# Kernel tuning notes

Measured on AMD Instinct MI355X. Metric: run time of the kernel, lower is better.

Reference implementation:

```python
import jax, jax.numpy as jnp
import numpy as np

B, S, F, E, H = 4, 2048, 512, 512, 8
DH = E // H


def setup_inputs() -> dict:
    key = jax.random.key(0)
    ks = jax.random.split(key, 8)
    sc = 1.0 / np.sqrt(F)
    return {
        "x": jax.random.normal(ks[0], (B, S, F), jnp.float32),
        "etype_emb": jax.random.normal(ks[1], (B, S, E), jnp.float32),
        "mask": jax.random.randint(ks[2], (B, S), 0, 2, jnp.int32),
        "Wq": jax.random.normal(ks[3], (F, E), jnp.float32) * sc,
        "bq": jnp.zeros((E,), jnp.float32),
        "Wk": jax.random.normal(ks[4], (F, E), jnp.float32) * sc,
        "bk": jnp.zeros((E,), jnp.float32),
        "Wv": jax.random.normal(ks[5], (F, E), jnp.float32) * sc,
        "bv": jnp.zeros((E,), jnp.float32),
    }


def _heads(t):
    # [B,S,E] -> [B,H,S,DH]; tf.split on last dim + concat on axis 1 == this reshape/transpose
    return t.reshape(B, S, H, DH).transpose(0, 2, 1, 3)


def reference(x, etype_emb, mask, Wq, bq, Wk, bk, Wv, bv):
    # Dropout is identity in inference mode (training=None)
    q = _heads(x @ Wq + bq + etype_emb)            # [B,H,S,DH]
    k = _heads(x @ Wk + bk)
    v = _heads(x @ Wv + bv)
    scores = jnp.einsum("bhqd,bhkd->bhqk", q, k) / jnp.sqrt(jnp.float32(DH))
    NEG = jnp.float32(-1e10)
    m = (mask == 1)
    # mask keys before softmax
    scores = jnp.where(m[:, None, None, :], scores, NEG)
    att = jax.nn.softmax(scores, axis=-1)
    # mask queries after softmax (zero out)
    att = jnp.where(m[:, None, :, None], att, jnp.float32(0.0))
    h = jnp.einsum("bhqk,bhkd->bhqd", att, v)       # [B,H,S,DH]
    return h.transpose(0, 2, 1, 3).reshape(B, S, E)
```

## Files before the change

### kernel.cpp

```cpp
#include <hip/hip_runtime.h>
#include <hip/hip_bf16.h>


typedef _Float16 f16x4 __attribute__((ext_vector_type(4)));
typedef _Float16 f16x8 __attribute__((ext_vector_type(8)));
typedef float f32x4 __attribute__((ext_vector_type(4)));

#define MFMA16(a, b, c) __builtin_amdgcn_mfma_f32_16x16x16f16((a), (b), (c), 0, 0, 0)
#define MFMA32(a, b, c) __builtin_amdgcn_mfma_f32_16x16x32_f16((a), (b), (c), 0, 0, 0)
#define GLDS16(g, l)                                                                     \
    __builtin_amdgcn_global_load_lds((const __attribute__((address_space(1))) void*)(g), \
                                     (__attribute__((address_space(3))) void*)(l), 16, 0, 0)

constexpr int Bn = 4, Sn = 2048, Fn = 512, En = 512, Hn = 8, DHn = 64;

__global__ void cvt_f32_to_f16(const float* __restrict__ in, _Float16* __restrict__ out, int n4) {
    int i = blockIdx.x * blockDim.x + threadIdx.x;
    int stride = gridDim.x * blockDim.x;
    for (; i < n4; i += stride) {
        float4 v = reinterpret_cast<const float4*>(in)[i];
        f16x4 o = { (_Float16)v.x, (_Float16)v.y, (_Float16)v.z, (_Float16)v.w };
        reinterpret_cast<f16x4*>(out)[i] = o;
    }
}

__global__ void cvt_wT(const float* __restrict__ Wq, const float* __restrict__ Wk,
                       const float* __restrict__ Wv, _Float16* __restrict__ out) {
    const int z = blockIdx.z;
    const float* W = (z == 0) ? Wq : ((z == 1) ? Wk : Wv);
    _Float16* o = out + (size_t)z * Fn * En;
    __shared__ float tile[16][17];
    int n = blockIdx.x * 16 + threadIdx.x;
    int k = blockIdx.y * 16 + threadIdx.y;
    tile[threadIdx.y][threadIdx.x] = W[k * En + n];
    __syncthreads();
    int n2 = blockIdx.x * 16 + threadIdx.y;
    int k2 = blockIdx.y * 16 + threadIdx.x;
    o[(size_t)n2 * Fn + k2] = (_Float16)tile[threadIdx.x][threadIdx.y];
}

__global__ __launch_bounds__(256) void qkv_gemm(
    const _Float16* __restrict__ xh, const _Float16* __restrict__ wT,
    const float* __restrict__ bq, const float* __restrict__ bk, const float* __restrict__ bv,
    char* __restrict__ Qh, char* __restrict__ Kpk, char* __restrict__ Vpk) {
    const int z = blockIdx.z;
    const _Float16* Wz = wT + (size_t)z * Fn * En;
    const float* bias = (z == 0) ? bq : ((z == 1) ? bk : bv);

    const int tid = threadIdx.x;
    const int wave = tid >> 6, lane = tid & 63;
    const int lr = lane & 15, hi = lane >> 4;
    const int wr = wave >> 1, wc = wave & 1;
    const int m0 = blockIdx.x * 128;
    const int n0 = blockIdx.y * 128;

    __shared__ __align__(16) char smem[34816];
    char* As = smem;
    char* Bs = smem + 16384;

    f32x4 acc[4][4] = {};

    const int inrow = (tid & 7) * 16;
    const int rowb = tid >> 3;

    const char* xg = (const char*)xh;
    const char* wg = (const char*)Wz;

    for (int t = 0; t < 8; ++t) {
        const int k0b = t * 128;
        __syncthreads();
#pragma unroll
        for (int it = 0; it < 4; ++it) {
            const int row = rowb + it * 32;
            const int srccol = inrow ^ ((row & 7) << 4);
            const char* ga = xg + (size_t)(m0 + row) * 1024 + k0b + srccol;
            const char* gb = wg + (size_t)(n0 + row) * 1024 + k0b + srccol;
            const int ldso = (it * 256 + tid) * 16;
            GLDS16(ga, As + ldso);
            GLDS16(gb, Bs + ldso);
        }
        asm volatile("s_waitcnt vmcnt(0)" ::: "memory");
        __syncthreads();
#pragma unroll
        for (int ks = 0; ks < 2; ++ks) {
            f16x8 af[4], bf[4];
            const int kb = ks * 64 + hi * 16;
#pragma unroll
            for (int mt = 0; mt < 4; ++mt) {
                const int row = wr * 64 + mt * 16 + lr;
                af[mt] = *reinterpret_cast<const f16x8*>(As + row * 128 + (kb ^ ((row & 7) << 4)));
            }
#pragma unroll
            for (int nt = 0; nt < 4; ++nt) {
                const int row = wc * 64 + nt * 16 + lr;
                bf[nt] = *reinterpret_cast<const f16x8*>(Bs + row * 128 + (kb ^ ((row & 7) << 4)));
            }
#pragma unroll
            for (int mt = 0; mt < 4; ++mt)
#pragma unroll
                for (int nt = 0; nt < 4; ++nt)
                    acc[mt][nt] = MFMA32(af[mt], bf[nt], acc[mt][nt]);
        }
    }

    __syncthreads();
    _Float16* tl = (_Float16*)smem;
    {
        const int cb = wc * 64 + lr;
#pragma unroll
        for (int mt = 0; mt < 4; ++mt) {
            const int sb = wr * 64 + mt * 16 + hi * 4;
#pragma unroll
            for (int nt = 0; nt < 4; ++nt) {
                const int c = cb + nt * 16;
                const float bz = bias[n0 + c];
#pragma unroll
                for (int r = 0; r < 4; ++r)
                    tl[(sb + r) * 136 + c] = (_Float16)(acc[mt][nt][r] + bz);
            }
        }
    }
    __syncthreads();

    const int b8 = (m0 >> 11) * 8;
    const int h0 = n0 >> 6;
    const int kt0 = (m0 & 2047) >> 6;
    char* outz = (z == 0) ? Qh : ((z == 1) ? Kpk : Vpk);

#pragma unroll
    for (int chunk = 0; chunk < 4; ++chunk) {
        const int hh = chunk >> 1, T = chunk & 1;
        char* base = outz + (size_t)(b8 + h0 + hh) * 262144 + (size_t)(kt0 + T) * 8192;
#pragma unroll
        for (int j = 0; j < 2; ++j) {
            const int g = tid * 16 + j * 4096;
            f16x8 val;
            if (z == 0) {
                const int s = T * 64 + (g >> 7), db = g & 127;
                val = *reinterpret_cast<const f16x8*>(&tl[s * 136 + hh * 64 + (db >> 1)]);
            } else if (z == 1) {
                const int r = g >> 7;
                const int colb = (g & 127) ^ ((r & 7) << 4);
                val = *reinterpret_cast<const f16x8*>(&tl[(T * 64 + r) * 136 + hh * 64 + (colb >> 1)]);
            } else {
                const int d = g >> 7;
                const int k0 = ((g & 127) ^ ((d & 7) << 4)) >> 1;
#pragma unroll
                for (int jj = 0; jj < 8; ++jj)
                    val[jj] = tl[(T * 64 + k0 + jj) * 136 + hh * 64 + d];
            }
            *reinterpret_cast<f16x8*>(base + g) = val;
        }
    }
}

__global__ __launch_bounds__(256, 4) void attn(
    const _Float16* __restrict__ Qh, const char* __restrict__ Kpk,
    const char* __restrict__ Vpk, const int* __restrict__ mask,
    const float* __restrict__ etype, float* __restrict__ out) {
    const int bid = blockIdx.x;
    const int bh = bid & 31, qb = bid >> 5;
    const int b = bh >> 3, h = bh & 7;
    const int tid = threadIdx.x;
    const int wave = tid >> 6, lane = tid & 63;
    const int lr = lane & 15, hi = lane >> 4;
    const int q0 = qb * 64 + wave * 16;

    const _Float16* Qb = Qh + (size_t)bh * Sn * DHn;
    const char* Kb = Kpk + (size_t)bh * 262144;
    const char* Vb = Vpk + (size_t)bh * 262144;
    const int* mb = mask + b * Sn;

    constexpr float CSC = 0.18033688011112042f;
    constexpr int NT = Sn / 64;

    __shared__ __align__(16) char kv[2][16384];

#pragma unroll
    for (int j = 0; j < 2; ++j) {
        GLDS16(Kb + tid * 16 + j * 4096, kv[0] + tid * 16 + j * 4096);
        GLDS16(Vb + tid * 16 + j * 4096, kv[0] + 8192 + tid * 16 + j * 4096);
    }

    f16x8 qf[2];
#pragma unroll
    for (int ks = 0; ks < 2; ++ks) {
        const f16x8 qh = *reinterpret_cast<const f16x8*>(Qb + (q0 + lr) * DHn + ks * 32 + hi * 8);
        const float* ep = etype + ((size_t)(b * Sn) + q0 + lr) * En + h * DHn + ks * 32 + hi * 8;
        const f32x4 e0 = *reinterpret_cast<const f32x4*>(ep);
        const f32x4 e1 = *reinterpret_cast<const f32x4*>(ep + 4);
        f16x8 q;
#pragma unroll
        for (int j = 0; j < 4; ++j) q[j] = (_Float16)(((float)qh[j] + e0[j]) * CSC);
#pragma unroll
        for (int j = 0; j < 4; ++j) q[4 + j] = (_Float16)(((float)qh[4 + j] + e1[j]) * CSC);
        qf[ks] = q;
    }

    f32x4 oaccT[4] = {};
    f32x4 osum = {};
    float mrun = -3e38f;
    const f16x4 onev = {(_Float16)1.f, (_Float16)1.f, (_Float16)1.f, (_Float16)1.f};

    asm volatile("s_waitcnt vmcnt(0)" ::: "memory");
    __syncthreads();

    for (int t = 0; t < NT; ++t) {
        const char* cbuf = kv[t & 1];
        char* nbuf = kv[(t + 1) & 1];

        const size_t nto = (size_t)((t + 1) & (NT - 1)) * 8192;
#pragma unroll
        for (int j = 0; j < 2; ++j) {
            GLDS16(Kb + nto + tid * 16 + j * 4096, nbuf + tid * 16 + j * 4096);
            GLDS16(Vb + nto + tid * 16 + j * 4096, nbuf + 8192 + tid * 16 + j * 4096);
        }

        const int key0 = t * 64;
        int4 km[4];
#pragma unroll
        for (int kt = 0; kt < 4; ++kt)
            km[kt] = *reinterpret_cast<const int4*>(mb + key0 + kt * 16 + hi * 4);

        f16x8 kf[4][2];
#pragma unroll
        for (int kt = 0; kt < 4; ++kt)
#pragma unroll
            for (int ks = 0; ks < 2; ++ks)
                kf[kt][ks] = *reinterpret_cast<const f16x8*>(
                    cbuf + (kt * 16 + lr) * 128 + ((ks * 64 + hi * 16) ^ ((lr & 7) << 4)));

        f32x4 scT[4] = {};
#pragma unroll
        for (int ks = 0; ks < 2; ++ks)
#pragma unroll
            for (int kt = 0; kt < 4; ++kt)
                scT[kt] = MFMA32(kf[kt][ks], qf[ks], scT[kt]);

        scT[0][0] = km[0].x ? scT[0][0] : -1e30f; scT[0][1] = km[0].y ? scT[0][1] : -1e30f;
        scT[0][2] = km[0].z ? scT[0][2] : -1e30f; scT[0][3] = km[0].w ? scT[0][3] : -1e30f;
        scT[1][0] = km[1].x ? scT[1][0] : -1e30f; scT[1][1] = km[1].y ? scT[1][1] : -1e30f;
        scT[1][2] = km[1].z ? scT[1][2] : -1e30f; scT[1][3] = km[1].w ? scT[1][3] : -1e30f;
        scT[2][0] = km[2].x ? scT[2][0] : -1e30f; scT[2][1] = km[2].y ? scT[2][1] : -1e30f;
        scT[2][2] = km[2].z ? scT[2][2] : -1e30f; scT[2][3] = km[2].w ? scT[2][3] : -1e30f;
        scT[3][0] = km[3].x ? scT[3][0] : -1e30f; scT[3][1] = km[3].y ? scT[3][1] : -1e30f;
        scT[3][2] = km[3].z ? scT[3][2] : -1e30f; scT[3][3] = km[3].w ? scT[3][3] : -1e30f;

        float mx = -3e38f;
#pragma unroll
        for (int kt = 0; kt < 4; ++kt)
#pragma unroll
            for (int r = 0; r < 4; ++r) mx = fmaxf(mx, scT[kt][r]);
        mx = fmaxf(mx, __shfl_xor(mx, 16));
        mx = fmaxf(mx, __shfl_xor(mx, 32));

        if (!__all(mx <= mrun + 8.0f)) {
            const float mnew = fmaxf(mrun, mx);
            const float al = exp2f(mrun - mnew);
            mrun = mnew;
#pragma unroll
            for (int dt = 0; dt < 4; ++dt) oaccT[dt] *= al;
            osum *= al;
        }

        f16x4 pa[4];
#pragma unroll
        for (int kt = 0; kt < 4; ++kt) {
            f16x4 p;
#pragma unroll
            for (int r = 0; r < 4; ++r) p[r] = (_Float16)exp2f(scT[kt][r] - mrun);
            pa[kt] = p;
        }

#pragma unroll
        for (int ks = 0; ks < 4; ++ks) {
#pragma unroll
            for (int dt = 0; dt < 4; ++dt) {
                const f16x4 vf = *reinterpret_cast<const f16x4*>(
                    cbuf + 8192 + (dt * 16 + lr) * 128 + ((ks * 32 + hi * 8) ^ ((lr & 7) << 4)));
                oaccT[dt] = MFMA16(vf, pa[ks], oaccT[dt]);
            }
            osum = MFMA16(onev, pa[ks], osum);
        }

        asm volatile("s_waitcnt vmcnt(0)" ::: "memory");
        __syncthreads();
    }

    const int srow = q0 + lr;
    const float inv = (mb[srow] != 0) ? 1.0f / osum[0] : 0.0f;
#pragma unroll
    for (int dt = 0; dt < 4; ++dt) {
        f32x4 o = oaccT[dt] * inv;
        *reinterpret_cast<f32x4*>(out + ((size_t)(b * Sn + srow)) * En + h * DHn + dt * 16 + hi * 4) = o;
    }
}

extern "C" void kernel_launch(void* const* d_in, const int* in_sizes, int n_in,
                              void* d_out, int out_size, void* d_ws, size_t ws_size,
                              hipStream_t stream) {
    const float* x = (const float*)d_in[0];
    const float* etype = (const float*)d_in[1];
    const int* mask = (const int*)d_in[2];
    const float* Wq = (const float*)d_in[3];
    const float* bq = (const float*)d_in[4];
    const float* Wk = (const float*)d_in[5];
    const float* bk = (const float*)d_in[6];
    const float* Wv = (const float*)d_in[7];
    const float* bv = (const float*)d_in[8];
    float* out = (float*)d_out;

    char* ws = (char*)d_ws;
    _Float16* xh = (_Float16*)(ws + 0);
    _Float16* wT = (_Float16*)(ws + 8388608);
    char* Qh = ws + 9961472;
    char* Kpk = ws + 18350080;
    char* Vpk = ws + 26738688;

    cvt_f32_to_f16<<<2048, 256, 0, stream>>>(x, xh, (Bn * Sn * Fn) / 4);
    cvt_wT<<<dim3(32, 32, 3), dim3(16, 16), 0, stream>>>(Wq, Wk, Wv, wT);
    qkv_gemm<<<dim3(64, 4, 3), 256, 0, stream>>>(xh, wT, bq, bk, bv, Qh, Kpk, Vpk);
    attn<<<1024, 256, 0, stream>>>((const _Float16*)Qh, Kpk, Vpk, mask, etype, out);
}
```

Measured before the change: 197.9 us.

## Pre-permute K/V fragment layout, cache additive mask in LDS, narrow QKV GEMM tiles

The QKV GEMM now uses 128x64 tiles (more blocks, launch bounds for 6 blocks/CU) with a swizzled LDS epilogue. K and V are written in the exact per-lane fragment order the attention MFMAs consume, so attention reads them with contiguous lane-indexed loads and no swizzle arithmetic. The key mask is loaded once into LDS as an additive 0/-1e30 bias that initializes the score accumulator, removing per-tile global mask loads and selects. The attention loop is unrolled by two to make double-buffer indices static. The risk is more LDS per attention block and a more complex store layout that must match the consumer exactly.

Result: faster. 189.9 us (-4.0%).

```diff
diff --git a/kernel.cpp b/kernel.cpp
--- a/kernel.cpp
+++ b/kernel.cpp
@@ -39,7 +39,7 @@
     o[(size_t)n2 * Fn + k2] = (_Float16)tile[threadIdx.x][threadIdx.y];
 }
 
-__global__ __launch_bounds__(256) void qkv_gemm(
+__global__ __launch_bounds__(256, 6) void qkv_gemm(
     const _Float16* __restrict__ xh, const _Float16* __restrict__ wT,
     const float* __restrict__ bq, const float* __restrict__ bk, const float* __restrict__ bv,
     char* __restrict__ Qh, char* __restrict__ Kpk, char* __restrict__ Vpk) {
@@ -50,19 +50,17 @@
     const int tid = threadIdx.x;
     const int wave = tid >> 6, lane = tid & 63;
     const int lr = lane & 15, hi = lane >> 4;
-    const int wr = wave >> 1, wc = wave & 1;
+    const int wr = wave >> 1, wn = wave & 1;
     const int m0 = blockIdx.x * 128;
-    const int n0 = blockIdx.y * 128;
-
-    __shared__ __align__(16) char smem[34816];
+    const int n0 = blockIdx.y * 64;
+
+    __shared__ __align__(16) char smem[24576];
     char* As = smem;
     char* Bs = smem + 16384;
 
-    f32x4 acc[4][4] = {};
-
+    f32x4 acc[4][2] = {};
     const int inrow = (tid & 7) * 16;
     const int rowb = tid >> 3;
-
     const char* xg = (const char*)xh;
     const char* wg = (const char*)Wz;
 
@@ -72,85 +70,84 @@
 #pragma unroll
         for (int it = 0; it < 4; ++it) {
             const int row = rowb + it * 32;
-            const int srccol = inrow ^ ((row & 7) << 4);
-            const char* ga = xg + (size_t)(m0 + row) * 1024 + k0b + srccol;
-            const char* gb = wg + (size_t)(n0 + row) * 1024 + k0b + srccol;
-            const int ldso = (it * 256 + tid) * 16;
-            GLDS16(ga, As + ldso);
-            GLDS16(gb, Bs + ldso);
+            const int sc = inrow ^ ((row & 7) << 4);
+            GLDS16(xg + (size_t)(m0 + row) * 1024 + k0b + sc, As + it * 4096 + tid * 16);
+            if (it < 2)
+                GLDS16(wg + (size_t)(n0 + row) * 1024 + k0b + sc, Bs + it * 4096 + tid * 16);
         }
         asm volatile("s_waitcnt vmcnt(0)" ::: "memory");
         __syncthreads();
 #pragma unroll
         for (int ks = 0; ks < 2; ++ks) {
-            f16x8 af[4], bf[4];
-            const int kb = ks * 64 + hi * 16;
-#pragma unroll
-            for (int mt = 0; mt < 4; ++mt) {
-                const int row = wr * 64 + mt * 16 + lr;
-                af[mt] = *reinterpret_cast<const f16x8*>(As + row * 128 + (kb ^ ((row & 7) << 4)));
-            }
-#pragma unroll
-            for (int nt = 0; nt < 4; ++nt) {
-                const int row = wc * 64 + nt * 16 + lr;
-                bf[nt] = *reinterpret_cast<const f16x8*>(Bs + row * 128 + (kb ^ ((row & 7) << 4)));
-            }
+            const int kb = (ks * 64 + hi * 16) ^ ((lr & 7) << 4);
+            f16x8 af[4], bf[2];
 #pragma unroll
             for (int mt = 0; mt < 4; ++mt)
-#pragma unroll
-                for (int nt = 0; nt < 4; ++nt)
+                af[mt] = *reinterpret_cast<const f16x8*>(As + (wr * 64 + mt * 16 + lr) * 128 + kb);
+#pragma unroll
+            for (int nt = 0; nt < 2; ++nt)
+                bf[nt] = *reinterpret_cast<const f16x8*>(Bs + (wn * 32 + nt * 16 + lr) * 128 + kb);
+#pragma unroll
+            for (int mt = 0; mt < 4; ++mt)
+#pragma unroll
+                for (int nt = 0; nt < 2; ++nt)
                     acc[mt][nt] = MFMA32(af[mt], bf[nt], acc[mt][nt]);
         }
     }
 
     __syncthreads();
-    _Float16* tl = (_Float16*)smem;
     {
-        const int cb = wc * 64 + lr;
+        const int cb = wn * 32 + lr;
 #pragma unroll
         for (int mt = 0; mt < 4; ++mt) {
             const int sb = wr * 64 + mt * 16 + hi * 4;
 #pragma unroll
-            for (int nt = 0; nt < 4; ++nt) {
+            for (int nt = 0; nt < 2; ++nt) {
                 const int c = cb + nt * 16;
                 const float bz = bias[n0 + c];
 #pragma unroll
-                for (int r = 0; r < 4; ++r)
-                    tl[(sb + r) * 136 + c] = (_Float16)(acc[mt][nt][r] + bz);
+                for (int r = 0; r < 4; ++r) {
+                    const int s = sb + r;
+                    *reinterpret_cast<_Float16*>(smem + s * 128 + ((c * 2) ^ ((s & 7) << 4))) =
+                        (_Float16)(acc[mt][nt][r] + bz);
+                }
             }
         }
     }
     __syncthreads();
 
-    const int b8 = (m0 >> 11) * 8;
-    const int h0 = n0 >> 6;
+    const int bb = m0 >> 11;
+    const int bh = bb * 8 + blockIdx.y;
     const int kt0 = (m0 & 2047) >> 6;
     char* outz = (z == 0) ? Qh : ((z == 1) ? Kpk : Vpk);
-
-#pragma unroll
-    for (int chunk = 0; chunk < 4; ++chunk) {
-        const int hh = chunk >> 1, T = chunk & 1;
-        char* base = outz + (size_t)(b8 + h0 + hh) * 262144 + (size_t)(kt0 + T) * 8192;
-#pragma unroll
-        for (int j = 0; j < 2; ++j) {
-            const int g = tid * 16 + j * 4096;
-            f16x8 val;
-            if (z == 0) {
-                const int s = T * 64 + (g >> 7), db = g & 127;
-                val = *reinterpret_cast<const f16x8*>(&tl[s * 136 + hh * 64 + (db >> 1)]);
-            } else if (z == 1) {
-                const int r = g >> 7;
-                const int colb = (g & 127) ^ ((r & 7) << 4);
-                val = *reinterpret_cast<const f16x8*>(&tl[(T * 64 + r) * 136 + hh * 64 + (colb >> 1)]);
-            } else {
-                const int d = g >> 7;
-                const int k0 = ((g & 127) ^ ((d & 7) << 4)) >> 1;
-#pragma unroll
-                for (int jj = 0; jj < 8; ++jj)
-                    val[jj] = tl[(T * 64 + k0 + jj) * 136 + hh * 64 + d];
-            }
-            *reinterpret_cast<f16x8*>(base + g) = val;
-        }
+    char* hb = outz + (size_t)bh * 262144 + (size_t)kt0 * 8192;
+    const char* sm = (const char*)smem;
+
+#pragma unroll
+    for (int j = 0; j < 4; ++j) {
+        const int g = tid * 16 + j * 4096;
+        const int T = g >> 13, g13 = g & 8191;
+        f16x8 val;
+        if (z == 0) {
+            const int s = T * 64 + (g13 >> 7);
+            val = *reinterpret_cast<const f16x8*>(sm + s * 128 + ((g13 & 127) ^ ((s & 7) << 4)));
+        } else if (z == 1) {
+            const int chunk = g13 >> 10, l2 = (g13 >> 4) & 63;
+            const int s = T * 64 + (chunk >> 1) * 16 + (l2 & 15);
+            const int db = (chunk & 1) * 64 + (l2 >> 4) * 16;
+            val = *reinterpret_cast<const f16x8*>(sm + s * 128 + (db ^ ((s & 7) << 4)));
+        } else {
+            const int chunk = g13 >> 10, l2 = (g13 >> 4) & 63;
+            const int ks = chunk >> 1, dp = chunk & 1;
+            const int lr2 = l2 & 15, hi2 = l2 >> 4;
+#pragma unroll
+            for (int i = 0; i < 8; ++i) {
+                const int d = (dp * 2 + (i >> 2)) * 16 + lr2;
+                const int s = T * 64 + ks * 16 + hi2 * 4 + (i & 3);
+                val[i] = *reinterpret_cast<const _Float16*>(sm + s * 128 + ((d * 2) ^ ((s & 7) << 4)));
+            }
+        }
+        *reinterpret_cast<f16x8*>(hb + g) = val;
     }
 }
 
@@ -168,20 +165,22 @@
 
     const _Float16* Qb = Qh + (size_t)bh * Sn * DHn;
     const char* Kb = Kpk + (size_t)bh * 262144;
-    const char* Vb = Vpk + (size_t)bh * 262144;
+    const char* Vg = Vpk + (size_t)bh * 262144;
     const int* mb = mask + b * Sn;
 
+    __shared__ __align__(16) char lds[40960];
+
+    {
+        const char* ms = (const char*)(mask + b * Sn);
+        GLDS16(ms + tid * 16, lds + 32768 + tid * 16);
+        GLDS16(ms + tid * 16 + 4096, lds + 32768 + tid * 16 + 4096);
+        GLDS16(Kb + tid * 16, lds + tid * 16);
+        GLDS16(Kb + tid * 16 + 4096, lds + tid * 16 + 4096);
+        GLDS16(Vg + tid * 16, lds + 8192 + tid * 16);
+        GLDS16(Vg + tid * 16 + 4096, lds + 8192 + tid * 16 + 4096);
+    }
+
     constexpr float CSC = 0.18033688011112042f;
-    constexpr int NT = Sn / 64;
-
-    __shared__ __align__(16) char kv[2][16384];
-
-#pragma unroll
-    for (int j = 0; j < 2; ++j) {
-        GLDS16(Kb + tid * 16 + j * 4096, kv[0] + tid * 16 + j * 4096);
-        GLDS16(Vb + tid * 16 + j * 4096, kv[0] + 8192 + tid * 16 + j * 4096);
-    }
-
     f16x8 qf[2];
 #pragma unroll
     for (int ks = 0; ks < 2; ++ks) {
@@ -205,86 +204,87 @@
     asm volatile("s_waitcnt vmcnt(0)" ::: "memory");
     __syncthreads();
 
-    for (int t = 0; t < NT; ++t) {
-        const char* cbuf = kv[t & 1];
-        char* nbuf = kv[(t + 1) & 1];
-
-        const size_t nto = (size_t)((t + 1) & (NT - 1)) * 8192;
-#pragma unroll
-        for (int j = 0; j < 2; ++j) {
-            GLDS16(Kb + nto + tid * 16 + j * 4096, nbuf + tid * 16 + j * 4096);
-            GLDS16(Vb + nto + tid * 16 + j * 4096, nbuf + 8192 + tid * 16 + j * 4096);
-        }
-
-        const int key0 = t * 64;
-        int4 km[4];
-#pragma unroll
-        for (int kt = 0; kt < 4; ++kt)
-            km[kt] = *reinterpret_cast<const int4*>(mb + key0 + kt * 16 + hi * 4);
-
-        f16x8 kf[4][2];
-#pragma unroll
-        for (int kt = 0; kt < 4; ++kt)
+    {
+        int4 a = *reinterpret_cast<const int4*>(lds + 32768 + tid * 16);
+        int4 c = *reinterpret_cast<const int4*>(lds + 32768 + tid * 16 + 4096);
+        __syncthreads();
+        f32x4 fa = {a.x ? 0.f : -1e30f, a.y ? 0.f : -1e30f, a.z ? 0.f : -1e30f, a.w ? 0.f : -1e30f};
+        f32x4 fc = {c.x ? 0.f : -1e30f, c.y ? 0.f : -1e30f, c.z ? 0.f : -1e30f, c.w ? 0.f : -1e30f};
+        *reinterpret_cast<f32x4*>(lds + 32768 + tid * 16) = fa;
+        *reinterpret_cast<f32x4*>(lds + 32768 + tid * 16 + 4096) = fc;
+        __syncthreads();
+    }
+
+    const char* kvr = lds + lane * 16;
+    const char* pmb = lds + 32768 + hi * 16;
+
+    for (int tp = 0; tp < 16; ++tp) {
+        const int tb = tp * 512;
+#pragma unroll
+        for (int u = 0; u < 2; ++u) {
+            const int t = tp * 2 + u;
+            const size_t nto = (size_t)((t + 1) & 31) * 8192;
+            char* nb = lds + (u ^ 1) * 16384;
+            GLDS16(Kb + nto + tid * 16, nb + tid * 16);
+            GLDS16(Kb + nto + tid * 16 + 4096, nb + tid * 16 + 4096);
+            GLDS16(Vg + nto + tid * 16, nb + 8192 + tid * 16);
+            GLDS16(Vg + nto + tid * 16 + 4096, nb + 8192 + tid * 16 + 4096);
+
+            f32x4 scT[4];
+#pragma unroll
+            for (int kt = 0; kt < 4; ++kt)
+                scT[kt] = *reinterpret_cast<const f32x4*>(pmb + tb + u * 256 + kt * 64);
+
+            const char* cb = kvr + u * 16384;
 #pragma unroll
             for (int ks = 0; ks < 2; ++ks)
-                kf[kt][ks] = *reinterpret_cast<const f16x8*>(
-                    cbuf + (kt * 16 + lr) * 128 + ((ks * 64 + hi * 16) ^ ((lr & 7) << 4)));
-
-        f32x4 scT[4] = {};
-#pragma unroll
-        for (int ks = 0; ks < 2; ++ks)
-#pragma unroll
-            for (int kt = 0; kt < 4; ++kt)
-                scT[kt] = MFMA32(kf[kt][ks], qf[ks], scT[kt]);
-
-        scT[0][0] = km[0].x ? scT[0][0] : -1e30f; scT[0][1] = km[0].y ? scT[0][1] : -1e30f;
-        scT[0][2] = km[0].z ? scT[0][2] : -1e30f; scT[0][3] = km[0].w ? scT[0][3] : -1e30f;
-        scT[1][0] = km[1].x ? scT[1][0] : -1e30f; scT[1][1] = km[1].y ? scT[1][1] : -1e30f;
-        scT[1][2] = km[1].z ? scT[1][2] : -1e30f; scT[1][3] = km[1].w ? scT[1][3] : -1e30f;
-        scT[2][0] = km[2].x ? scT[2][0] : -1e30f; scT[2][1] = km[2].y ? scT[2][1] : -1e30f;
-        scT[2][2] = km[2].z ? scT[2][2] : -1e30f; scT[2][3] = km[2].w ? scT[2][3] : -1e30f;
-        scT[3][0] = km[3].x ? scT[3][0] : -1e30f; scT[3][1] = km[3].y ? scT[3][1] : -1e30f;
-        scT[3][2] = km[3].z ? scT[3][2] : -1e30f; scT[3][3] = km[3].w ? scT[3][3] : -1e30f;
-
-        float mx = -3e38f;
-#pragma unroll
-        for (int kt = 0; kt < 4; ++kt)
-#pragma unroll
-            for (int r = 0; r < 4; ++r) mx = fmaxf(mx, scT[kt][r]);
-        mx = fmaxf(mx, __shfl_xor(mx, 16));
-        mx = fmaxf(mx, __shfl_xor(mx, 32));
-
-        if (!__all(mx <= mrun + 8.0f)) {
-            const float mnew = fmaxf(mrun, mx);
-            const float al = exp2f(mrun - mnew);
-            mrun = mnew;
-#pragma unroll
-            for (int dt = 0; dt < 4; ++dt) oaccT[dt] *= al;
-            osum *= al;
-        }
-
-        f16x4 pa[4];
-#pragma unroll
-        for (int kt = 0; kt < 4; ++kt) {
-            f16x4 p;
-#pragma unroll
-            for (int r = 0; r < 4; ++r) p[r] = (_Float16)exp2f(scT[kt][r] - mrun);
-            pa[kt] = p;
-        }
-
-#pragma unroll
-        for (int ks = 0; ks < 4; ++ks) {
-#pragma unroll
-            for (int dt = 0; dt < 4; ++dt) {
-                const f16x4 vf = *reinterpret_cast<const f16x4*>(
-                    cbuf + 8192 + (dt * 16 + lr) * 128 + ((ks * 32 + hi * 8) ^ ((lr & 7) << 4)));
-                oaccT[dt] = MFMA16(vf, pa[ks], oaccT[dt]);
-            }
-            osum = MFMA16(onev, pa[ks], osum);
-        }
-
-        asm volatile("s_waitcnt vmcnt(0)" ::: "memory");
-        __syncthreads();
+#pragma unroll
+                for (int kt = 0; kt < 4; ++kt) {
+                    const f16x8 kf = *reinterpret_cast<const f16x8*>(cb + (kt * 2 + ks) * 1024);
+                    scT[kt] = MFMA32(kf, qf[ks], scT[kt]);
+                }
+
+            float mx = fmaxf(fmaxf(scT[0][0], scT[0][1]), fmaxf(scT[0][2], scT[0][3]));
+            mx = fmaxf(mx, fmaxf(fmaxf(scT[1][0], scT[1][1]), fmaxf(scT[1][2], scT[1][3])));
+            mx = fmaxf(mx, fmaxf(fmaxf(scT[2][0], scT[2][1]), fmaxf(scT[2][2], scT[2][3])));
+            mx = fmaxf(mx, fmaxf(fmaxf(scT[3][0], scT[3][1]), fmaxf(scT[3][2], scT[3][3])));
+            mx = fmaxf(mx, __shfl_xor(mx, 16));
+            mx = fmaxf(mx, __shfl_xor(mx, 32));
+
+            if (!__all(mx <= mrun + 8.0f)) {
+                const float mnew = fmaxf(mrun, mx);
+                const float al = exp2f(mrun - mnew);
+                mrun = mnew;
+#pragma unroll
+                for (int dt = 0; dt < 4; ++dt) oaccT[dt] *= al;
+                osum *= al;
+            }
+
+            f16x4 pa[4];
+#pragma unroll
+            for (int kt = 0; kt < 4; ++kt) {
+                f16x4 p;
+#pragma unroll
+                for (int r = 0; r < 4; ++r) p[r] = (_Float16)exp2f(scT[kt][r] - mrun);
+                pa[kt] = p;
+            }
+
+#pragma unroll
+            for (int ks = 0; ks < 4; ++ks) {
+#pragma unroll
+                for (int dp = 0; dp < 2; ++dp) {
+                    const f16x8 vv = *reinterpret_cast<const f16x8*>(cb + 8192 + (ks * 2 + dp) * 1024);
+                    const f16x4 v0 = {vv[0], vv[1], vv[2], vv[3]};
+                    const f16x4 v1 = {vv[4], vv[5], vv[6], vv[7]};
+                    oaccT[dp * 2] = MFMA16(v0, pa[ks], oaccT[dp * 2]);
+                    oaccT[dp * 2 + 1] = MFMA16(v1, pa[ks], oaccT[dp * 2 + 1]);
+                }
+                osum = MFMA16(onev, pa[ks], osum);
+            }
+
+            asm volatile("s_waitcnt vmcnt(0)" ::: "memory");
+            __syncthreads();
+        }
     }
 
     const int srow = q0 + lr;
@@ -319,6 +319,6 @@
 
     cvt_f32_to_f16<<<2048, 256, 0, stream>>>(x, xh, (Bn * Sn * Fn) / 4);
     cvt_wT<<<dim3(32, 32, 3), dim3(16, 16), 0, stream>>>(Wq, Wk, Wv, wT);
-    qkv_gemm<<<dim3(64, 4, 3), 256, 0, stream>>>(xh, wT, bq, bk, bv, Qh, Kpk, Vpk);
+    qkv_gemm<<<dim3(64, 8, 3), 256, 0, stream>>>(xh, wT, bq, bk, bv, Qh, Kpk, Vpk);
     attn<<<1024, 256, 0, stream>>>((const _Float16*)Qh, Kpk, Vpk, mask, etype, out);
 }
```
